# Performance work log

Hardware: AMD Instinct MI355X
Metric: run time of the kernel (lower is better)

The kernel has to match this reference:

```python
import jax, jax.numpy as jnp
import numpy as np

D_MODEL = 1024
SEL_DIM = 64
CONFIGS = [(4, 32), (8, 64), (16, 128)]  # (heads, dim)
B, T = 2, 2048


def setup_inputs() -> dict:
    key = jax.random.key(0)
    ks = jax.random.split(key, 20)
    s = 0.02  # init scale for stability
    inp = {
        "x": jax.random.normal(ks[0], (B, T, D_MODEL), jnp.float32),
        "sel_w1": jax.random.normal(ks[1], (SEL_DIM, D_MODEL), jnp.float32) * s,
        "sel_b1": jnp.zeros((SEL_DIM,), jnp.float32),
        "sel_w2": jax.random.normal(ks[2], (SEL_DIM, SEL_DIM), jnp.float32) * s,
        "sel_b2": jnp.zeros((SEL_DIM,), jnp.float32),
        "sel_w3": jax.random.normal(ks[3], (len(CONFIGS), SEL_DIM), jnp.float32) * s,
        "sel_b3": jnp.zeros((len(CONFIGS),), jnp.float32),
    }
    for i, (h, d) in enumerate(CONFIGS):
        inp[f"qw{i}"] = jax.random.normal(ks[4 + 3 * i], (h * d, D_MODEL), jnp.float32) * s
        inp[f"kw{i}"] = jax.random.normal(ks[5 + 3 * i], (d, D_MODEL), jnp.float32) * s
        inp[f"ww{i}"] = jax.random.normal(ks[6 + 3 * i], (h, D_MODEL), jnp.float32) * s
    return inp


def _seq_features(x):
    # x: [b,t,d]
    b, t, d = x.shape
    seq_mean = jnp.mean(x, axis=1, keepdims=True)            # [b,1,d]
    seq_std = jnp.std(x, axis=1, keepdims=True, ddof=1)      # torch.std is unbiased
    pos = (jnp.arange(t, dtype=x.dtype) / t)[None, :, None]  # [1,t,1] broadcast to [b,t,d]
    return x + seq_mean + seq_std + pos * 0.1


def _forward(x, sel_w1, sel_b1, sel_w2, sel_b2, sel_w3, sel_b3,
             qw0, kw0, ww0, qw1, kw1, ww1, qw2, kw2, ww2):
    b, t, dm = x.shape
    feats = _seq_features(x)
    h1 = jax.nn.relu(feats @ sel_w1.T + sel_b1)
    h2 = jax.nn.relu(h1 @ sel_w2.T + sel_b2)
    config_probs = jax.nn.softmax(h2 @ sel_w3.T + sel_b3, axis=-1)  # [b,t,ncfg]

    per_cfg = [(qw0, kw0, ww0), (qw1, kw1, ww1), (qw2, kw2, ww2)]
    final = jnp.zeros((b, t, t), dtype=x.dtype)
    for i, ((heads, dim), (qw, kw, ww)) in enumerate(zip(CONFIGS, per_cfg)):
        q = (x @ qw.T).reshape(b, t, heads, dim)   # [b,t,h,d]
        k = x @ kw.T                               # [b,s,d]
        w = x @ ww.T                               # [b,t,h]
        dots = jnp.einsum('bthd,bsd->bths', q, k)  # [b,t,h,s]
        score = jnp.einsum('bths,bth->bts', jax.nn.relu(dots), w)  # relu*weight, sum heads
        final = final + config_probs[:, :, i:i + 1] * score
    return final


def reference(x, sel_w1, sel_b1, sel_w2, sel_b2, sel_w3, sel_b3,
              qw0, kw0, ww0, qw1, kw1, ww1, qw2, kw2, ww2):
    return _forward(x, sel_w1, sel_b1, sel_w2, sel_b2, sel_w3, sel_b3,
                    qw0, kw0, ww0, qw1, kw1, ww1, qw2, kw2, ww2)
```

## Files before the change

kernel.cpp:

```cpp
#include <hip/hip_runtime.h>
#include <cstdint>
#include <cstddef>
#include <math.h>

#define B_ 2
#define T_ 2048
#define D_ 1024
#define M_ (B_*T_)

#define QO0 0
#define KO0 128
#define WO0 160
#define QO1 168
#define KO1 680
#define WO1 744
#define QO2 752
#define KO2 2800
#define WO2 2928
#define SELO 2944
#define LDN 3072

typedef float f32x16 __attribute__((ext_vector_type(16)));
typedef short bf16x8 __attribute__((ext_vector_type(8)));
typedef unsigned short u16;

__device__ __forceinline__ u16 f2bf(float f) {
    unsigned int u = __float_as_uint(f);
    unsigned int r = (u + 0x7fffu + ((u >> 16) & 1u)) >> 16;
    return (u16)r;
}
__device__ __forceinline__ float bf2f(u16 b) {
    return __uint_as_float(((unsigned int)b) << 16);
}

__device__ __forceinline__ void gload16(const void* g, void* l) {
    __builtin_amdgcn_global_load_lds(
        (const __attribute__((address_space(1))) unsigned int*)g,
        (__attribute__((address_space(3))) unsigned int*)l,
        16, 0, 0);
}

__device__ __forceinline__ void stage_plane(const u16* src_base, int row_stride, int k0,
                                            int rg, int lane, u16* dst) {
    int row = rg * 16 + (lane >> 2);
    const u16* s = src_base + (size_t)row * row_stride + k0 + (lane & 3) * 8;
    gload16(s, dst + rg * 512);
}

__global__ void stats_partial(const float* __restrict__ x,
                              float* __restrict__ part, float* __restrict__ part2) {
    int d  = blockIdx.x * 256 + threadIdx.x;
    int tc = blockIdx.y;
    int b  = blockIdx.z;
    const float* p = x + (size_t)b * T_ * D_ + (size_t)tc * 128 * D_ + d;
    float s = 0.f, s2 = 0.f;
    for (int t = 0; t < 128; ++t) {
        float v = p[(size_t)t * D_];
        s += v; s2 += v * v;
    }
    part [(b * 16 + tc) * D_ + d] = s;
    part2[(b * 16 + tc) * D_ + d] = s2;
}

__global__ void stats_final(const float* __restrict__ part, const float* __restrict__ part2,
                            float* __restrict__ ms) {
    int idx = blockIdx.x * 256 + threadIdx.x;
    if (idx >= B_ * D_) return;
    int b = idx / D_, d = idx % D_;
    float s = 0.f, s2 = 0.f;
    for (int i = 0; i < 16; ++i) {
        s  += part [(b * 16 + i) * D_ + d];
        s2 += part2[(b * 16 + i) * D_ + d];
    }
    float mean = s / (float)T_;
    float var  = (s2 - (float)T_ * mean * mean) / (float)(T_ - 1);
    ms[idx] = mean + sqrtf(fmaxf(var, 0.f));
}

__global__ void msdot(const float* __restrict__ ms, const float* __restrict__ w1,
                      float* __restrict__ msd, float* __restrict__ s1) {
    int b = blockIdx.x, j = threadIdx.x;
    const float* wr = w1 + (size_t)j * D_;
    const float* mr = ms + (size_t)b * D_;
    float am = 0.f, as = 0.f;
    for (int d4 = 0; d4 < D_ / 4; ++d4) {
        float4 w = *(const float4*)(wr + d4 * 4);
        float4 m = *(const float4*)(mr + d4 * 4);
        am += w.x * m.x + w.y * m.y + w.z * m.z + w.w * m.w;
        as += w.x + w.y + w.z + w.w;
    }
    msd[b * 64 + j] = am;
    if (b == 0) s1[j] = as;
}

__global__ void split_w(const float* __restrict__ qw0, const float* __restrict__ kw0,
                        const float* __restrict__ ww0, const float* __restrict__ qw1,
                        const float* __restrict__ kw1, const float* __restrict__ ww1,
                        const float* __restrict__ qw2, const float* __restrict__ kw2,
                        const float* __restrict__ ww2, const float* __restrict__ w1s,
                        u16* __restrict__ Wh) {
    int row = blockIdx.x;
    int col = threadIdx.x * 4;
    const float* src = nullptr;
    if      (row < 128)  src = qw0 + (size_t)row * D_;
    else if (row < 160)  src = kw0 + (size_t)(row - 128) * D_;
    else if (row < 164)  src = ww0 + (size_t)(row - 160) * D_;
    else if (row < 168)  src = nullptr;
    else if (row < 680)  src = qw1 + (size_t)(row - 168) * D_;
    else if (row < 744)  src = kw1 + (size_t)(row - 680) * D_;
    else if (row < 752)  src = ww1 + (size_t)(row - 744) * D_;
    else if (row < 2800) src = qw2 + (size_t)(row - 752) * D_;
    else if (row < 2928) src = kw2 + (size_t)(row - 2800) * D_;
    else if (row < 2944) src = ww2 + (size_t)(row - 2928) * D_;
    else if (row < 3008) src = w1s + (size_t)(row - 2944) * D_;
    float4 v = src ? *(const float4*)(src + col) : make_float4(0.f, 0.f, 0.f, 0.f);
    ushort4 h;
    h.x = f2bf(v.x); h.y = f2bf(v.y); h.z = f2bf(v.z); h.w = f2bf(v.w);
    *(ushort4*)&Wh[(size_t)row * D_ + col] = h;
}

__global__ void split_x(const float* __restrict__ x, u16* __restrict__ Xh, u16* __restrict__ Xl) {
    size_t i = ((size_t)blockIdx.x * 256 + threadIdx.x) * 4;
    float4 v = *(const float4*)(x + i);
    float vv[4] = {v.x, v.y, v.z, v.w};
    ushort4 h, l;
    u16 hb;
    hb = f2bf(vv[0]); h.x = hb; l.x = f2bf(vv[0] - bf2f(hb));
    hb = f2bf(vv[1]); h.y = hb; l.y = f2bf(vv[1] - bf2f(hb));
    hb = f2bf(vv[2]); h.z = hb; l.z = f2bf(vv[2] - bf2f(hb));
    hb = f2bf(vv[3]); h.w = hb; l.w = f2bf(vv[3] - bf2f(hb));
    *(ushort4*)&Xh[i] = h;
    *(ushort4*)&Xl[i] = l;
}

__global__ __launch_bounds__(256, 3) void proj_gemm(
    const u16* __restrict__ Xh, const u16* __restrict__ Xl, const u16* __restrict__ Wh,
    u16* __restrict__ Ph) {
    __shared__ u16 Ah[2][4096], Al[2][4096], Bh[2][4096];
    int tid = threadIdx.x;
    int wave = tid >> 6, lane = tid & 63;
    int bm = blockIdx.x * 128, bn = blockIdx.y * 128;
    int wt = wave >> 1, wn = wave & 1;
    int fm = lane & 31, half8 = (lane >> 5) * 8;
    f32x16 acc[2][2];
#pragma unroll
    for (int i = 0; i < 2; ++i)
#pragma unroll
        for (int j = 0; j < 2; ++j)
#pragma unroll
            for (int r = 0; r < 16; ++r) acc[i][j][r] = 0.f;

    const u16* xh = Xh + (size_t)bm * D_;
    const u16* xl = Xl + (size_t)bm * D_;
    const u16* wh = Wh + (size_t)bn * D_;

    auto stage = [&](int buf, int k0) {
        for (int j = wave; j < 24; j += 4) {
            int pl = j >> 3, rg = j & 7;
            if      (pl == 0) stage_plane(xh, D_, k0, rg, lane, Ah[buf]);
            else if (pl == 1) stage_plane(xl, D_, k0, rg, lane, Al[buf]);
            else              stage_plane(wh, D_, k0, rg, lane, Bh[buf]);
        }
    };

    stage(0, 0);
    for (int kc = 0; kc < 32; ++kc) {
        __syncthreads();
        if (kc + 1 < 32) stage((kc + 1) & 1, (kc + 1) * 32);
        const u16* ah = Ah[kc & 1];
        const u16* al = Al[kc & 1];
        const u16* bh = Bh[kc & 1];
#pragma unroll
        for (int ks = 0; ks < 2; ++ks) {
            int fk = ks * 16 + half8;
            bf16x8 a_h[2], a_l[2], b_h[2];
#pragma unroll
            for (int t = 0; t < 2; ++t) {
                a_h[t] = *(const bf16x8*)&ah[(wt * 64 + t * 32 + fm) * 32 + fk];
                a_l[t] = *(const bf16x8*)&al[(wt * 64 + t * 32 + fm) * 32 + fk];
                b_h[t] = *(const bf16x8*)&bh[(wn * 64 + t * 32 + fm) * 32 + fk];
            }
#pragma unroll
            for (int ti = 0; ti < 2; ++ti)
#pragma unroll
                for (int tj = 0; tj < 2; ++tj) {
                    acc[ti][tj] = __builtin_amdgcn_mfma_f32_32x32x16_bf16(a_h[ti], b_h[tj], acc[ti][tj], 0, 0, 0);
                    acc[ti][tj] = __builtin_amdgcn_mfma_f32_32x32x16_bf16(a_l[ti], b_h[tj], acc[ti][tj], 0, 0, 0);
                }
        }
    }
#pragma unroll
    for (int ti = 0; ti < 2; ++ti)
#pragma unroll
        for (int tj = 0; tj < 2; ++tj)
#pragma unroll
            for (int r = 0; r < 16; ++r) {
                int row = bm + wt * 64 + ti * 32 + (r & 3) + 8 * (r >> 2) + 4 * (lane >> 5);
                int col = bn + wn * 64 + tj * 32 + (lane & 31);
                Ph[(size_t)row * LDN + col] = f2bf(acc[ti][tj][r]);
            }
}

__global__ void selector2(const u16* __restrict__ Ph,
                          const float* __restrict__ msd, const float* __restrict__ s1,
                          const float* __restrict__ b1, const float* __restrict__ w2,
                          const float* __restrict__ b2, const float* __restrict__ w3,
                          const float* __restrict__ b3, float* __restrict__ PR) {
    __shared__ float h1s[4][64];
    __shared__ float h2s[4][64];
    __shared__ float lg[4][3];
    int tid = threadIdx.x;
    int slot = tid >> 6, j = tid & 63;
    int bt = blockIdx.x * 4 + slot;
    int b = bt >> 11, t = bt & 2047;
    size_t pidx = (size_t)bt * LDN + SELO + j;
    float v = bf2f(Ph[pidx])
            + msd[b * 64 + j] + 0.1f * ((float)t / (float)T_) * s1[j] + b1[j];
    h1s[slot][j] = fmaxf(v, 0.f);
    __syncthreads();
    float a2 = b2[j];
#pragma unroll 8
    for (int d = 0; d < 64; ++d) a2 = fmaf(h1s[slot][d], w2[j * 64 + d], a2);
    h2s[slot][j] = fmaxf(a2, 0.f);
    __syncthreads();
    if (j < 3) {
        float a3 = b3[j];
        for (int d = 0; d < 64; ++d) a3 = fmaf(h2s[slot][d], w3[j * 64 + d], a3);
        lg[slot][j] = a3;
    }
    __syncthreads();
    if (j == 0) {
        float m = fmaxf(lg[slot][0], fmaxf(lg[slot][1], lg[slot][2]));
        float e0 = expf(lg[slot][0] - m), e1 = expf(lg[slot][1] - m), e2 = expf(lg[slot][2] - m);
        float inv = 1.f / (e0 + e1 + e2);
        PR[bt * 3 + 0] = e0 * inv;
        PR[bt * 3 + 1] = e1 * inv;
        PR[bt * 3 + 2] = e2 * inv;
    }
}

__device__ __forceinline__ int qcol_of(int c) {
    if (c < 2)  return QO0 + c * 64;
    if (c < 10) return QO1 + (c - 2) * 64;
    int u = c - 10;
    return QO2 + (u >> 1) * 128 + (u & 1) * 64;
}

__global__ __launch_bounds__(256, 2) void score_kernel(
    const u16* __restrict__ Ph, const float* __restrict__ PR, float* __restrict__ out) {
    __shared__ u16 Qs[2][8192];
    __shared__ u16 Ks[4 * 4096];
    __shared__ float wpT[28 * 128];
    int tid = threadIdx.x;
    int wave = tid >> 6, lane = tid & 63;
    int wt = wave >> 1, wn = wave & 1;
    int fm = lane & 31, half8 = (lane >> 5) * 8;

    int n = blockIdx.z * 256 + blockIdx.y * 16 + blockIdx.x;
    int p = (n & 7) * 4 + (n >> 7);
    int xb = (n >> 3) & 15;
    int b = p >> 4, yb = p & 15;
    int t0 = yb * 128, s0 = xb * 128;

    const u16* Pq = Ph + (size_t)(b * T_ + t0) * LDN;
    const u16* Pk = Ph + (size_t)(b * T_ + s0) * LDN;

    auto stageQ = [&](int buf, int qcol) {
#pragma unroll
        for (int i = 0; i < 4; ++i) {
            int j = (wave << 2) + i;
            int pl = j >> 3, rg = j & 7;
            stage_plane(Pq, LDN, qcol + pl * 32, rg, lane, &Qs[buf][pl * 4096]);
        }
    };
    auto stageK = [&](int kbase, int nplanes) {
        for (int j = wave; j < nplanes * 8; j += 4) {
            int pl = j >> 3, rg = j & 7;
            stage_plane(Pk, LDN, kbase + pl * 32, rg, lane, &Ks[pl * 4096]);
        }
    };

    stageK(KO0, 1);
    stageQ(0, qcol_of(0));

    for (int idx = tid; idx < 28 * 128; idx += 256) {
        int g = idx >> 7, r = idx & 127;
        int wcol = (g < 4) ? (WO0 + g) : ((g < 12) ? (WO1 + g - 4) : (WO2 + g - 12));
        int cfg  = (g < 4) ? 0 : ((g < 12) ? 1 : 2);
        size_t prow = (size_t)(b * T_ + t0 + r);
        wpT[g * 128 + r] = bf2f(Ph[prow * LDN + wcol]) * PR[prow * 3 + cfg];
    }

    f32x16 outacc[2][2], dots[2][2];
#pragma unroll
    for (int i = 0; i < 2; ++i)
#pragma unroll
        for (int j = 0; j < 2; ++j)
#pragma unroll
            for (int r = 0; r < 16; ++r) { outacc[i][j][r] = 0.f; dots[i][j][r] = 0.f; }

    for (int c = 0; c < 42; ++c) {
        int kp0, kp1, gMid, gEnd;
        if (c < 2)       { kp0 = 0; kp1 = 0; gMid = 2 * c; gEnd = 2 * c + 1; }
        else if (c < 10) { kp0 = 0; kp1 = 1; gMid = -1; gEnd = 4 + (c - 2); }
        else { int u = c - 10; int h = u >> 1, kb = u & 1;
               kp0 = kb * 2; kp1 = kb * 2 + 1; gMid = -1; gEnd = kb ? (12 + h) : -1; }

        __syncthreads();
        if (c < 41) stageQ((c + 1) & 1, qcol_of(c + 1));

        const u16* qb = Qs[c & 1];
#pragma unroll
        for (int ks = 0; ks < 4; ++ks) {
            int fcol = (ks & 1) * 16 + half8;
            int kp = (ks < 2) ? kp0 : kp1;
            bf16x8 kf[2], qf[2];
#pragma unroll
            for (int tj = 0; tj < 2; ++tj)
                kf[tj] = *(const bf16x8*)&Ks[kp * 4096 + (wn * 64 + tj * 32 + fm) * 32 + fcol];
#pragma unroll
            for (int ti = 0; ti < 2; ++ti)
                qf[ti] = *(const bf16x8*)&qb[(ks >> 1) * 4096 + (wt * 64 + ti * 32 + fm) * 32 + fcol];
#pragma unroll
            for (int ti = 0; ti < 2; ++ti)
#pragma unroll
                for (int tj = 0; tj < 2; ++tj)
                    dots[ti][tj] = __builtin_amdgcn_mfma_f32_32x32x16_bf16(qf[ti], kf[tj], dots[ti][tj], 0, 0, 0);

            int g = (ks == 1) ? gMid : ((ks == 3) ? gEnd : -1);
            if (g >= 0) {
#pragma unroll
                for (int ti = 0; ti < 2; ++ti) {
                    int rowbase = wt * 64 + ti * 32 + 4 * (lane >> 5);
#pragma unroll
                    for (int rq = 0; rq < 4; ++rq) {
                        float4 w4 = *(const float4*)&wpT[g * 128 + rowbase + rq * 8];
                        float wv[4] = {w4.x, w4.y, w4.z, w4.w};
#pragma unroll
                        for (int tj = 0; tj < 2; ++tj)
#pragma unroll
                            for (int r2 = 0; r2 < 4; ++r2) {
                                int r = rq * 4 + r2;
                                outacc[ti][tj][r] += fmaxf(dots[ti][tj][r], 0.f) * wv[r2];
                                dots[ti][tj][r] = 0.f;
                            }
                    }
                }
            }
        }
        if (c == 1)      { __syncthreads(); stageK(KO1, 2); }
        else if (c == 9) { __syncthreads(); stageK(KO2, 4); }
    }

#pragma unroll
    for (int ti = 0; ti < 2; ++ti)
#pragma unroll
        for (int tj = 0; tj < 2; ++tj)
#pragma unroll
            for (int r = 0; r < 16; ++r) {
                int trow = wt * 64 + ti * 32 + (r & 3) + 8 * (r >> 2) + 4 * (lane >> 5);
                int scol = wn * 64 + tj * 32 + (lane & 31);
                out[(size_t)(b * T_ + t0 + trow) * T_ + (s0 + scol)] = outacc[ti][tj][r];
            }
}

extern "C" void kernel_launch(void* const* d_in, const int* in_sizes, int n_in,
                              void* d_out, int out_size, void* d_ws, size_t ws_size,
                              hipStream_t stream) {
    const float* x   = (const float*)d_in[0];
    const float* w1  = (const float*)d_in[1];
    const float* b1  = (const float*)d_in[2];
    const float* w2  = (const float*)d_in[3];
    const float* b2  = (const float*)d_in[4];
    const float* w3  = (const float*)d_in[5];
    const float* b3  = (const float*)d_in[6];
    const float* qw0 = (const float*)d_in[7];
    const float* kw0 = (const float*)d_in[8];
    const float* ww0 = (const float*)d_in[9];
    const float* qw1 = (const float*)d_in[10];
    const float* kw1 = (const float*)d_in[11];
    const float* ww1 = (const float*)d_in[12];
    const float* qw2 = (const float*)d_in[13];
    const float* kw2 = (const float*)d_in[14];
    const float* ww2 = (const float*)d_in[15];
    float* out = (float*)d_out;

    float* fb = (float*)d_ws;
    float* MS  = fb; fb += 2048;
    float* MSD = fb; fb += 128;
    float* S1  = fb; fb += 64;
    float* PR  = fb; fb += (size_t)M_ * 3;
    float* PA  = fb; fb += (size_t)B_ * 16 * D_;
    float* PA2 = fb; fb += (size_t)B_ * 16 * D_;
    u16* ub = (u16*)fb;
    u16* Wh = ub; ub += (size_t)LDN * D_;
    u16* Xh = ub; ub += (size_t)M_ * D_;
    u16* Xl = ub; ub += (size_t)M_ * D_;
    u16* Ph = ub; ub += (size_t)M_ * LDN;

    stats_partial<<<dim3(D_ / 256, 16, B_), 256, 0, stream>>>(x, PA, PA2);
    stats_final<<<dim3((B_ * D_ + 255) / 256), 256, 0, stream>>>(PA, PA2, MS);
    msdot<<<dim3(B_), 64, 0, stream>>>(MS, w1, MSD, S1);
    split_w<<<dim3(LDN), 256, 0, stream>>>(qw0, kw0, ww0, qw1, kw1, ww1,
                                           qw2, kw2, ww2, w1, Wh);
    split_x<<<dim3((M_ * D_) / 1024), 256, 0, stream>>>(x, Xh, Xl);
    proj_gemm<<<dim3(M_ / 128, LDN / 128), 256, 0, stream>>>(Xh, Xl, Wh, Ph);
    selector2<<<dim3(M_ / 4), 256, 0, stream>>>(Ph, MSD, S1, b1, w2, b2, w3, b3, PR);
    score_kernel<<<dim3(T_ / 128, T_ / 128, B_), 256, 0, stream>>>(Ph, PR, out);
}
```

Baseline: 296.7 us.

## Drop bf16 low-part split of x and swizzle LDS tiles to avoid bank conflicts

The projection GEMM no longer represents x as a high plus low bf16 pair. It casts x once to bf16, which halves the MFMA count, the LDS footprint and the staging traffic in proj_gemm, and it raises occupancy to 4 blocks. Separately, the LDS staging layout is XOR-swizzled on 16-byte slots, and both proj_gemm and score_kernel fragment reads are remapped to match, to reduce bank conflicts. The risk is lower precision in the projections, which feed relu(dots) and the selector.

```diff
diff --git a/kernel.cpp b/kernel.cpp
--- a/kernel.cpp
+++ b/kernel.cpp
@@ -42,8 +42,10 @@
 
 __device__ __forceinline__ void stage_plane(const u16* src_base, int row_stride, int k0,
                                             int rg, int lane, u16* dst) {
-    int row = rg * 16 + (lane >> 2);
-    const u16* s = src_base + (size_t)row * row_stride + k0 + (lane & 3) * 8;
+    int rl  = lane >> 2;
+    int row = rg * 16 + rl;
+    int q   = (lane & 3) ^ (rl & 3) ^ ((rl >> 2) & 3);
+    const u16* s = src_base + (size_t)row * row_stride + k0 + q * 8;
     gload16(s, dst + rg * 512);
 }
 
@@ -119,29 +121,23 @@
     *(ushort4*)&Wh[(size_t)row * D_ + col] = h;
 }
 
-__global__ void split_x(const float* __restrict__ x, u16* __restrict__ Xh, u16* __restrict__ Xl) {
+__global__ void cast_x(const float* __restrict__ x, u16* __restrict__ Xh) {
     size_t i = ((size_t)blockIdx.x * 256 + threadIdx.x) * 4;
     float4 v = *(const float4*)(x + i);
-    float vv[4] = {v.x, v.y, v.z, v.w};
-    ushort4 h, l;
-    u16 hb;
-    hb = f2bf(vv[0]); h.x = hb; l.x = f2bf(vv[0] - bf2f(hb));
-    hb = f2bf(vv[1]); h.y = hb; l.y = f2bf(vv[1] - bf2f(hb));
-    hb = f2bf(vv[2]); h.z = hb; l.z = f2bf(vv[2] - bf2f(hb));
-    hb = f2bf(vv[3]); h.w = hb; l.w = f2bf(vv[3] - bf2f(hb));
+    ushort4 h;
+    h.x = f2bf(v.x); h.y = f2bf(v.y); h.z = f2bf(v.z); h.w = f2bf(v.w);
     *(ushort4*)&Xh[i] = h;
-    *(ushort4*)&Xl[i] = l;
-}
-
-__global__ __launch_bounds__(256, 3) void proj_gemm(
-    const u16* __restrict__ Xh, const u16* __restrict__ Xl, const u16* __restrict__ Wh,
-    u16* __restrict__ Ph) {
-    __shared__ u16 Ah[2][4096], Al[2][4096], Bh[2][4096];
+}
+
+__global__ __launch_bounds__(256, 4) void proj_gemm(
+    const u16* __restrict__ Xh, const u16* __restrict__ Wh, u16* __restrict__ Ph) {
+    __shared__ u16 As[2][4096], Bs[2][4096];
     int tid = threadIdx.x;
     int wave = tid >> 6, lane = tid & 63;
     int bm = blockIdx.x * 128, bn = blockIdx.y * 128;
     int wt = wave >> 1, wn = wave & 1;
-    int fm = lane & 31, half8 = (lane >> 5) * 8;
+    int fm = lane & 31, hv = lane >> 5;
+    int tkey = (fm & 3) ^ ((fm >> 2) & 3);
     f32x16 acc[2][2];
 #pragma unroll
     for (int i = 0; i < 2; ++i)
@@ -151,15 +147,14 @@
             for (int r = 0; r < 16; ++r) acc[i][j][r] = 0.f;
 
     const u16* xh = Xh + (size_t)bm * D_;
-    const u16* xl = Xl + (size_t)bm * D_;
     const u16* wh = Wh + (size_t)bn * D_;
 
     auto stage = [&](int buf, int k0) {
-        for (int j = wave; j < 24; j += 4) {
+#pragma unroll
+        for (int i = 0; i < 4; ++i) {
+            int j = wave * 4 + i;
             int pl = j >> 3, rg = j & 7;
-            if      (pl == 0) stage_plane(xh, D_, k0, rg, lane, Ah[buf]);
-            else if (pl == 1) stage_plane(xl, D_, k0, rg, lane, Al[buf]);
-            else              stage_plane(wh, D_, k0, rg, lane, Bh[buf]);
+            stage_plane(pl ? wh : xh, D_, k0, rg, lane, pl ? Bs[buf] : As[buf]);
         }
     };
 
@@ -167,26 +162,22 @@
     for (int kc = 0; kc < 32; ++kc) {
         __syncthreads();
         if (kc + 1 < 32) stage((kc + 1) & 1, (kc + 1) * 32);
-        const u16* ah = Ah[kc & 1];
-        const u16* al = Al[kc & 1];
-        const u16* bh = Bh[kc & 1];
+        const u16* ah = As[kc & 1];
+        const u16* bh = Bs[kc & 1];
 #pragma unroll
         for (int ks = 0; ks < 2; ++ks) {
-            int fk = ks * 16 + half8;
-            bf16x8 a_h[2], a_l[2], b_h[2];
+            int slot8 = ((ks * 2 + hv) ^ tkey) * 8;
+            bf16x8 a_h[2], b_h[2];
 #pragma unroll
             for (int t = 0; t < 2; ++t) {
-                a_h[t] = *(const bf16x8*)&ah[(wt * 64 + t * 32 + fm) * 32 + fk];
-                a_l[t] = *(const bf16x8*)&al[(wt * 64 + t * 32 + fm) * 32 + fk];
-                b_h[t] = *(const bf16x8*)&bh[(wn * 64 + t * 32 + fm) * 32 + fk];
+                a_h[t] = *(const bf16x8*)&ah[(wt * 64 + t * 32 + fm) * 32 + slot8];
+                b_h[t] = *(const bf16x8*)&bh[(wn * 64 + t * 32 + fm) * 32 + slot8];
             }
 #pragma unroll
             for (int ti = 0; ti < 2; ++ti)
 #pragma unroll
-                for (int tj = 0; tj < 2; ++tj) {
+                for (int tj = 0; tj < 2; ++tj)
                     acc[ti][tj] = __builtin_amdgcn_mfma_f32_32x32x16_bf16(a_h[ti], b_h[tj], acc[ti][tj], 0, 0, 0);
-                    acc[ti][tj] = __builtin_amdgcn_mfma_f32_32x32x16_bf16(a_l[ti], b_h[tj], acc[ti][tj], 0, 0, 0);
-                }
         }
     }
 #pragma unroll
@@ -254,7 +245,8 @@
     int tid = threadIdx.x;
     int wave = tid >> 6, lane = tid & 63;
     int wt = wave >> 1, wn = wave & 1;
-    int fm = lane & 31, half8 = (lane >> 5) * 8;
+    int fm = lane & 31, hv = lane >> 5;
+    int tkey = (fm & 3) ^ ((fm >> 2) & 3);
 
     int n = blockIdx.z * 256 + blockIdx.y * 16 + blockIdx.x;
     int p = (n & 7) * 4 + (n >> 7);
@@ -312,15 +304,15 @@
         const u16* qb = Qs[c & 1];
 #pragma unroll
         for (int ks = 0; ks < 4; ++ks) {
-            int fcol = (ks & 1) * 16 + half8;
+            int slot8 = (((ks & 1) * 2 + hv) ^ tkey) * 8;
             int kp = (ks < 2) ? kp0 : kp1;
             bf16x8 kf[2], qf[2];
 #pragma unroll
             for (int tj = 0; tj < 2; ++tj)
-                kf[tj] = *(const bf16x8*)&Ks[kp * 4096 + (wn * 64 + tj * 32 + fm) * 32 + fcol];
+                kf[tj] = *(const bf16x8*)&Ks[kp * 4096 + (wn * 64 + tj * 32 + fm) * 32 + slot8];
 #pragma unroll
             for (int ti = 0; ti < 2; ++ti)
-                qf[ti] = *(const bf16x8*)&qb[(ks >> 1) * 4096 + (wt * 64 + ti * 32 + fm) * 32 + fcol];
+                qf[ti] = *(const bf16x8*)&qb[(ks >> 1) * 4096 + (wt * 64 + ti * 32 + fm) * 32 + slot8];
 #pragma unroll
             for (int ti = 0; ti < 2; ++ti)
 #pragma unroll
@@ -395,7 +387,6 @@
     u16* ub = (u16*)fb;
     u16* Wh = ub; ub += (size_t)LDN * D_;
     u16* Xh = ub; ub += (size_t)M_ * D_;
-    u16* Xl = ub; ub += (size_t)M_ * D_;
     u16* Ph = ub; ub += (size_t)M_ * LDN;
 
     stats_partial<<<dim3(D_ / 256, 16, B_), 256, 0, stream>>>(x, PA, PA2);
@@ -403,8 +394,8 @@
     msdot<<<dim3(B_), 64, 0, stream>>>(MS, w1, MSD, S1);
     split_w<<<dim3(LDN), 256, 0, stream>>>(qw0, kw0, ww0, qw1, kw1, ww1,
                                            qw2, kw2, ww2, w1, Wh);
-    split_x<<<dim3((M_ * D_) / 1024), 256, 0, stream>>>(x, Xh, Xl);
-    proj_gemm<<<dim3(M_ / 128, LDN / 128), 256, 0, stream>>>(Xh, Xl, Wh, Ph);
+    cast_x<<<dim3((M_ * D_) / 1024), 256, 0, stream>>>(x, Xh);
+    proj_gemm<<<dim3(M_ / 128, LDN / 128), 256, 0, stream>>>(Xh, Wh, Ph);
     selector2<<<dim3(M_ / 4), 256, 0, stream>>>(Ph, MSD, S1, b1, w2, b2, w3, b3, PR);
     score_kernel<<<dim3(T_ / 128, T_ / 128, B_), 256, 0, stream>>>(Ph, PR, out);
 }
```

Result: faster. 273.5 us (-7.8%).
